# Optimization experiments

Hardware: AMD Instinct MI355X
Metric: run time of the kernel (lower is better)

## Reference

```python
import jax, jax.numpy as jnp
import numpy as np

N_CLASS = 20
N_SIGMA = 2
H = W = 512
B = 4
N_INST = 32
W_INST, W_VAR, W_SEED = 1.0, 10.0, 1.0
FG_WEIGHT = 10.0


def _xym():
    # channel 0: x along width, channel 1: y along height (matches torch buffer)
    xm = jnp.broadcast_to(jnp.linspace(0.0, 1.0, W)[None, :], (H, W))
    ym = jnp.broadcast_to(jnp.linspace(0.0, 1.0, H)[:, None], (H, W))
    return jnp.stack([xm, ym], axis=0)  # [2, H, W]


def lovasz_hinge_flat(logits, gt, valid):
    # logits, gt (0/1 float), valid (bool), all flat [P]; ignored pixels excluded
    P = logits.shape[0]
    vf = valid.astype(logits.dtype)
    signs = 2.0 * gt - 1.0
    # push ignored pixels to the end of the descending sort; relu(-1e9)=0 kills them
    errors = jnp.where(valid, 1.0 - logits * signs, -1e9)
    errors_sorted, perm = jax.lax.top_k(errors, P)  # descending
    gt_sorted = jnp.take(gt * vf, perm)
    v_sorted = jnp.take(vf, perm)
    gts = jnp.sum(gt * vf)
    inter = gts - jnp.cumsum(gt_sorted)
    union = gts + jnp.cumsum((1.0 - gt_sorted) * v_sorted)
    jac = 1.0 - inter / jnp.maximum(union, 1e-9)
    jac = jnp.concatenate([jac[:1], jac[1:] - jac[:-1]])
    return jnp.sum(jax.nn.relu(errors_sorted) * jac)


def _per_image(pred_b, inst_b, lab_b, xym, fg_w, n_inst):
    spatial_emb = jnp.tanh(pred_b[:2]) + xym            # [2,H,W]
    sigma = pred_b[2:2 + N_SIGMA]                       # [n_sigma,H,W]
    seed = jax.nn.sigmoid(pred_b[2 + N_SIGMA:2 + N_SIGMA + N_CLASS])  # [C,H,W]
    inst = inst_b[0]
    lab = lab_b[0]
    valid = (lab != 255)

    # background seed loss: sum over classes of seed^2 on pixels not of that class
    cls_ids = jnp.arange(N_CLASS)
    bg = (lab[None] != (cls_ids + 1)[:, None, None]) & valid[None]
    seed_bg = jnp.sum(jnp.square(seed) * bg)

    def per_inst(iid):
        m = (inst == iid)
        mf = m.astype(pred_b.dtype)
        cnt = jnp.maximum(jnp.sum(mf), 1.0)
        # to_center=True: center is mean coordinate of instance pixels
        center = jnp.sum(xym * mf[None], axis=(1, 2)) / cnt          # [2]
        s_mean = jnp.sum(sigma * mf[None], axis=(1, 2)) / cnt        # [n_sigma]
        var_l = jnp.sum(jnp.square(sigma - jax.lax.stop_gradient(s_mean)[:, None, None]) * mf[None]) / (N_SIGMA * cnt)
        s = jnp.exp(s_mean * 10.0)
        dist = jnp.exp(-jnp.sum(jnp.square(spatial_emb - center[:, None, None]) * s[:, None, None], axis=0))  # [H,W]
        inst_l = lovasz_hinge_flat((dist * 2.0 - 1.0).reshape(-1), mf.reshape(-1), valid.reshape(-1))
        cls = jnp.max(lab * m) - 1  # instance class (0-indexed)
        seed_c = jnp.take(seed, cls, axis=0)
        seed_fg = jnp.take(fg_w, cls) * jnp.sum(jnp.square(seed_c - jax.lax.stop_gradient(dist)) * mf)
        return inst_l, var_l, seed_fg

    inst_ls, var_ls, seed_fgs = jax.vmap(per_inst)(jnp.arange(1, n_inst + 1))
    instance_loss = jnp.sum(inst_ls) / n_inst
    var_loss = jnp.sum(var_ls) / n_inst
    seed_loss = (seed_bg + jnp.sum(seed_fgs)) / (H * W)
    return W_INST * instance_loss + W_VAR * var_loss + W_SEED * seed_loss


def setup_inputs() -> dict:
    key = jax.random.key(0)
    k1, k2 = jax.random.split(key)
    prediction = jax.random.normal(k1, (B, 2 + N_SIGMA + N_CLASS, H, W), dtype=jnp.float32)
    instances = jax.random.randint(k2, (B, 1, H, W), 0, N_INST + 1).astype(jnp.int32)
    # each instance id has a consistent class, as the torch instance_to_cls dict assumes
    labels = jnp.where(instances > 0, ((instances - 1) % N_CLASS) + 1, 0).astype(jnp.int32)
    return {"prediction": prediction, "instances": instances, "labels": labels, "n_instances": N_INST}


def reference(prediction, instances, labels, n_instances):
    xym = _xym()
    fg_w = jnp.full((N_CLASS,), FG_WEIGHT, dtype=prediction.dtype)
    per = jax.vmap(lambda p, i, l: _per_image(p, i, l, xym, fg_w, n_instances))(prediction, instances, labels)
    return jnp.mean(per) + jnp.sum(prediction) * 0.0
```

## Files before the change

### kernel.cpp

```cpp
#include <hip/hip_runtime.h>
#include <hip/hip_fp16.h>
#include <math.h>

#define HH 512
#define WW 512
#define BB 4
#define NCLS 20
#define NINST 32
#define NPIX (HH*WW)
#define NCH 24
#define NBIN 128
#define NCHUNK3 256
#define CPX3 1024
#define K3T 512
#define HSTR 33

#define OFF_PARTA  ((size_t)0)
#define OFF_PSEED  (OFF_PARTA + 1024*256*4)
#define OFF_STATS  (OFF_PSEED + 1024*4)
#define OFF_DER    (OFF_STATS + 8*128*4)
#define OFF_SEEDBG (OFF_DER + 7*128*4)
#define OFF_INSTL  (OFF_SEEDBG + 4*4)
#define OFF_SFG    (OFF_INSTL + 128*4)
#define OFF_REC    ((OFF_SFG + 1024*4 + 255) & ~(size_t)255)
#define OFF_HIST   (OFF_REC + (size_t)BB*NPIX*8)

__device__ __forceinline__ float fast_rcp(float x) { return __builtin_amdgcn_rcpf(x); }
__device__ __forceinline__ float fast_sigmoid(float z) { return fast_rcp(1.0f + __expf(-z)); }
__device__ __forceinline__ float fast_tanh(float x) {
  return 1.0f - 2.0f * fast_rcp(__expf(2.0f * x) + 1.0f);
}

__global__ __launch_bounds__(256) void k1_stats(
    const float* __restrict__ pred, const int* __restrict__ inst,
    const int* __restrict__ lab,
    float* __restrict__ partA, float* __restrict__ partSeed,
    uint2* __restrict__ rec)
{
  __shared__ unsigned s_st[4][NINST][9];
  __shared__ float s_seed;
  int t = threadIdx.x;
  int w = t >> 6;
  for (int i = t; i < 4*NINST*9; i += 256) ((unsigned*)s_st)[i] = 0u;
  if (t == 0) s_seed = 0.f;
  __syncthreads();

  int b = blockIdx.x >> 8;
  int blk = blockIdx.x & 255;
  const float* pb = pred + (size_t)b*NCH*NPIX;
  float seedloc = 0.f;

  int p = blk*1024 + t*4;
  float4 e0v = *(const float4*)(pb + p);
  float4 e1v = *(const float4*)(pb + NPIX + p);
  float4 g0v = *(const float4*)(pb + 2*NPIX + p);
  float4 g1v = *(const float4*)(pb + 3*NPIX + p);
  int4 idv = *(const int4*)(inst + (size_t)b*NPIX + p);
  int4 lbv = *(const int4*)(lab + (size_t)b*NPIX + p);

  #pragma unroll
  for (int u = 0; u < 4; ++u) {
    int px = p + u;
    int x = px & (WW-1);
    int y = px >> 9;
    float xm = x * (1.0f/(WW-1));
    float ym = y * (1.0f/(HH-1));
    float g0 = (&g0v.x)[u];
    float g1 = (&g1v.x)[u];
    int id = (&idv.x)[u];
    int lb = (&lbv.x)[u];
    if (id >= 1) {
      int j = id - 1;
      unsigned* row = s_st[w][j];
      atomicAdd(&row[0], 1u | ((lb != 255) ? 0x10000u : 0u));
      atomicAdd((float*)&row[1], xm);
      atomicAdd((float*)&row[2], ym);
      atomicAdd((float*)&row[3], g0);
      atomicAdd((float*)&row[4], g1);
      atomicAdd((float*)&row[5], g0*g0);
      atomicAdd((float*)&row[6], g1*g1);
    }
  }

  float so[4] = {0.f,0.f,0.f,0.f};
  float Sv[4] = {0.f,0.f,0.f,0.f};
  for (int c = 0; c < NCLS; ++c) {
    float4 sv = *(const float4*)(pb + (size_t)(4+c)*NPIX + p);
    #pragma unroll
    for (int u = 0; u < 4; ++u) {
      float sg = fast_sigmoid((&sv.x)[u]);
      Sv[u] += sg*sg;
      if (c + 1 == (&lbv.x)[u]) so[u] = sg;
    }
  }
  #pragma unroll
  for (int u = 0; u < 4; ++u)
    if ((&lbv.x)[u] != 255) seedloc += Sv[u] - so[u]*so[u];

  {
    uint2 r4[4];
    #pragma unroll
    for (int u = 0; u < 4; ++u) {
      int px = p + u;
      int x = px & (WW-1);
      int y = px >> 9;
      float ex = fast_tanh((&e0v.x)[u]) + x * (1.0f/(WW-1));
      float ey = fast_tanh((&e1v.x)[u]) + y * (1.0f/(HH-1));
      __half2 h = __floats2half2_rn(ex, ey);
      unsigned valid = ((&lbv.x)[u] != 255) ? 1u : 0u;
      unsigned meta = (unsigned)(&idv.x)[u] | (valid << 7);
      r4[u].x = *reinterpret_cast<unsigned*>(&h);
      r4[u].y = (unsigned)(unsigned char)(so[u]*255.f + 0.5f) | (meta << 8);
    }
    uint4* dst = (uint4*)(rec + (size_t)b*NPIX + p);
    dst[0] = make_uint4(r4[0].x, r4[0].y, r4[1].x, r4[1].y);
    dst[1] = make_uint4(r4[2].x, r4[2].y, r4[3].x, r4[3].y);
  }

  for (int o = 32; o; o >>= 1) seedloc += __shfl_down(seedloc, o);
  if ((t & 63) == 0) atomicAdd(&s_seed, seedloc);
  __syncthreads();

  {
    int j = t & 31, f = t >> 5;
    float v;
    if (f == 0) {
      unsigned s = (s_st[0][j][0] & 0xFFFFu) + (s_st[1][j][0] & 0xFFFFu)
                 + (s_st[2][j][0] & 0xFFFFu) + (s_st[3][j][0] & 0xFFFFu);
      v = (float)s;
    } else if (f == 7) {
      unsigned s = (s_st[0][j][0] >> 16) + (s_st[1][j][0] >> 16)
                 + (s_st[2][j][0] >> 16) + (s_st[3][j][0] >> 16);
      v = (float)s;
    } else {
      v = __uint_as_float(s_st[0][j][f]) + __uint_as_float(s_st[1][j][f])
        + __uint_as_float(s_st[2][j][f]) + __uint_as_float(s_st[3][j][f]);
    }
    partA[(blockIdx.x << 8) + t] = v;
  }
  if (t == 0) partSeed[blockIdx.x] = s_seed;
}

__global__ __launch_bounds__(256) void k2a_reduce(
    const float* __restrict__ partA, float* __restrict__ stats)
{
  __shared__ float red[256];
  int bid = blockIdx.x;
  int b = bid >> 3, f = bid & 7;
  int t = threadIdx.x;
  int j = t & 31, grp = t >> 5;
  float s = 0.f;
  #pragma unroll 8
  for (int k = 0; k < 32; ++k) {
    int blk = grp*32 + k;
    s += partA[((b*256 + blk) << 8) + (f << 5) + j];
  }
  red[t] = s; __syncthreads();
  for (int st = 128; st >= 32; st >>= 1) {
    if (t < st) red[t] += red[t + st];
    __syncthreads();
  }
  if (t < 32) stats[f*128 + b*32 + t] = red[t];
}

__global__ __launch_bounds__(128) void k2b_derive(
    const float* __restrict__ stats, const float* __restrict__ partSeed,
    float* __restrict__ der, float* __restrict__ seedbg)
{
  int t = threadIdx.x;
  if (t < 4) {
    float ss = 0.f;
    for (int i = 0; i < 256; ++i) ss += partSeed[t*256 + i];
    seedbg[t] = ss;
  }
  float cntA = stats[0*128+t];
  float cnt = fmaxf(cntA, 1.0f);
  float sumx = stats[1*128+t], sumy = stats[2*128+t];
  float s0 = stats[3*128+t], s1 = stats[4*128+t];
  float q0 = stats[5*128+t], q1 = stats[6*128+t];
  float Gv = stats[7*128+t];
  float cx = sumx/cnt, cy = sumy/cnt;
  float sm0 = s0/cnt, sm1 = s1/cnt;
  float varnum = q0 - 2.f*sm0*s0 + cntA*sm0*sm0
               + q1 - 2.f*sm1*s1 + cntA*sm1*sm1;
  float varl = varnum / (2.0f * cnt);
  der[0*128+t] = cx;
  der[1*128+t] = cy;
  der[2*128+t] = -1.442695041f * expf(10.f*sm0);
  der[3*128+t] = -1.442695041f * expf(10.f*sm1);
  der[4*128+t] = varl;
  der[5*128+t] = Gv;
}

__global__ __launch_bounds__(K3T) void k3_hist(
    const uint2* __restrict__ rec, const float* __restrict__ der,
    unsigned* __restrict__ hist, float* __restrict__ sfg)
{
  __shared__ unsigned hc[NBIN*HSTR];
  __shared__ float s_fg[8];
  int t = threadIdx.x;
  for (int i = t; i < NBIN*HSTR; i += K3T) hc[i] = 0u;
  int bid = blockIdx.x;
  int b = bid >> 8;
  int chunk = bid & 255;
  int w = t >> 6, lane = t & 63;
  int j = lane & 31, jp1 = j + 1;
  int pair = b*NINST + j;
  float cx = der[0*128+pair], cy = der[1*128+pair];
  float s0 = der[2*128+pair], s1 = der[3*128+pair];
  const uint2* rb = rec + (size_t)b*NPIX + chunk*CPX3 + w*128;
  __syncthreads();

  float fg = 0.f;
  #pragma unroll 4
  for (int r = 0; r < 64; ++r) {
    uint2 rv = rb[r*2 + (lane >> 5)];
    __half2 h;
    *reinterpret_cast<unsigned*>(&h) = rv.x;
    float2 e = __half22float2(h);
    unsigned hi = rv.y;
    float dx = e.x - cx, dy = e.y - cy;
    float dist = exp2f(dx*dx*s0 + dy*dy*s1);
    bool own = ((int)((hi >> 8) & 0x3F) == jp1);
    if (own) { float d = (float)(hi & 0xFFu)*(1.0f/255.f) - dist; fg += d*d; }
    if (hi & 0x8000u) {
      float f = own ? (1.0f - dist) : dist;
      unsigned bin = min((unsigned)(f * (float)NBIN), NBIN-1u);
      atomicAdd(&hc[bin*HSTR + j], own ? 0x10001u : 1u);
    }
  }
  for (int o = 32; o; o >>= 1) fg += __shfl_down(fg, o);
  if (lane == 0) s_fg[w] = fg;
  __syncthreads();
  if (t == 0) {
    float s = 0.f;
    #pragma unroll
    for (int i = 0; i < 8; ++i) s += s_fg[i];
    sfg[bid] = 10.0f * s;
  }
  unsigned* out = hist + (size_t)(b*NCHUNK3 + chunk) * (NINST*NBIN);
  #pragma unroll
  for (int k = 0; k < NINST*NBIN/K3T; ++k) {
    int idx = k*K3T + t;
    out[idx] = hc[(idx & 127)*HSTR + (idx >> 7)];
  }
}

__global__ __launch_bounds__(512) void k4_scan(
    const unsigned* __restrict__ hist, const float* __restrict__ der,
    float* __restrict__ instl)
{
  __shared__ unsigned s_c[4][NBIN], s_p[4][NBIN];
  int t = threadIdx.x;
  int pair = blockIdx.x;
  int b = pair >> 5, j = pair & 31;
  int grp = t >> 7, bin = t & 127;
  const unsigned* bp = hist + ((size_t)b*NCHUNK3*NINST + j)*NBIN + bin;
  unsigned c = 0, p = 0;
  #pragma unroll 8
  for (int ch = grp*64; ch < grp*64 + 64; ++ch) {
    unsigned v = bp[(size_t)ch * (NINST*NBIN)];
    c += v & 0xFFFFu; p += v >> 16;
  }
  s_c[grp][bin] = c; s_p[grp][bin] = p;
  __syncthreads();
  if (t < NBIN) {
    s_c[0][t] += s_c[1][t] + s_c[2][t] + s_c[3][t];
    s_p[0][t] += s_p[1][t] + s_p[2][t] + s_p[3][t];
  }
  __syncthreads();

  if (t < 64) {
    int lane = t;
    float G = der[5*128+pair];
    unsigned carryN = 0, carryP = 0;
    float Jprev = 0.f, L = 0.f;
    for (int c8 = 0; c8 < NBIN/64; ++c8) {
      int k = NBIN - 1 - c8*64 - lane;
      unsigned n = s_c[0][k], pp0 = s_p[0][k];
      for (int off = 1; off < 64; off <<= 1) {
        unsigned nn = __shfl_up(n, off);
        unsigned pq = __shfl_up(pp0, off);
        if (lane >= off) { n += nn; pp0 += pq; }
      }
      float fN = (float)(carryN + n);
      float fP = (float)(carryP + pp0);
      float uni = G + fN - fP;
      float J = 1.0f - (G - fP) / fmaxf(uni, 1e-9f);
      float Jp = __shfl_up(J, 1);
      if (lane == 0) Jp = Jprev;
      float v = (k + 0.5f) * (2.0f/NBIN);
      L += v * (J - Jp);
      carryN += __shfl(n, 63);
      carryP += __shfl(pp0, 63);
      Jprev  = __shfl(J, 63);
    }
    for (int o = 32; o; o >>= 1) L += __shfl_down(L, o);
    if (lane == 0) instl[pair] = L;
  }
}

__global__ __launch_bounds__(256) void k5_final(
    const float* __restrict__ instl, const float* __restrict__ der,
    const float* __restrict__ seedbg, const float* __restrict__ sfg,
    float* __restrict__ out)
{
  __shared__ float red[256];
  int t = threadIdx.x;
  float acc = 0.f;
  for (int i = t; i < 1024; i += 256) acc += sfg[i];
  acc *= (1.0f/NPIX);
  if (t < 4) acc += seedbg[t] * (1.0f/NPIX);
  if (t < 128) acc += (instl[t] + 10.0f*der[4*128+t]) * (1.0f/NINST);
  red[t] = acc; __syncthreads();
  for (int s = 128; s; s >>= 1) { if (t < s) red[t] += red[t+s]; __syncthreads(); }
  if (t == 0) out[0] = red[0] * (1.0f/BB);
}

extern "C" void kernel_launch(void* const* d_in, const int* in_sizes, int n_in,
                              void* d_out, int out_size, void* d_ws, size_t ws_size,
                              hipStream_t stream)
{
  const float* pred = (const float*)d_in[0];
  const int* inst = (const int*)d_in[1];
  const int* lab  = (const int*)d_in[2];
  char* ws = (char*)d_ws;
  float* partA = (float*)(ws + OFF_PARTA);
  float* partSeed = (float*)(ws + OFF_PSEED);
  float* stats = (float*)(ws + OFF_STATS);
  float* der = (float*)(ws + OFF_DER);
  float* seedbg = (float*)(ws + OFF_SEEDBG);
  float* instl = (float*)(ws + OFF_INSTL);
  float* sfg = (float*)(ws + OFF_SFG);
  uint2* rec = (uint2*)(ws + OFF_REC);
  unsigned* hist = (unsigned*)(ws + OFF_HIST);

  hipLaunchKernelGGL(k1_stats, dim3(1024), dim3(256), 0, stream,
                     pred, inst, lab, partA, partSeed, rec);
  hipLaunchKernelGGL(k2a_reduce, dim3(32), dim3(256), 0, stream, partA, stats);
  hipLaunchKernelGGL(k2b_derive, dim3(1), dim3(128), 0, stream,
                     stats, partSeed, der, seedbg);
  hipLaunchKernelGGL(k3_hist, dim3(BB*NCHUNK3), dim3(K3T), 0, stream,
                     rec, der, hist, sfg);
  hipLaunchKernelGGL(k4_scan, dim3(128), dim3(512), 0, stream, hist, der, instl);
  hipLaunchKernelGGL(k5_final, dim3(1), dim3(256), 0, stream,
                     instl, der, seedbg, sfg, (float*)d_out);
}
```

Measured before the change: 94.01 us.

## Fuse derive and final kernels, skip bin-zero histogram atomics

```diff
diff --git a/kernel.cpp b/kernel.cpp
--- a/kernel.cpp
+++ b/kernel.cpp
@@ -17,12 +17,13 @@
 
 #define OFF_PARTA  ((size_t)0)
 #define OFF_PSEED  (OFF_PARTA + 1024*256*4)
-#define OFF_STATS  (OFF_PSEED + 1024*4)
-#define OFF_DER    (OFF_STATS + 8*128*4)
-#define OFF_SEEDBG (OFF_DER + 7*128*4)
-#define OFF_INSTL  (OFF_SEEDBG + 4*4)
+#define OFF_STATS  (OFF_PSEED + 1024*8)
+#define OFF_SEEDBG (OFF_STATS + 8*128*4)
+#define OFF_VALID  (OFF_SEEDBG + 4*4)
+#define OFF_INSTL  (OFF_VALID + 4*4)
 #define OFF_SFG    (OFF_INSTL + 128*4)
-#define OFF_REC    ((OFF_SFG + 1024*4 + 255) & ~(size_t)255)
+#define OFF_CNT    (OFF_SFG + 1024*4)
+#define OFF_REC    ((OFF_CNT + 4 + 255) & ~(size_t)255)
 #define OFF_HIST   (OFF_REC + (size_t)BB*NPIX*8)
 
 __device__ __forceinline__ float fast_rcp(float x) { return __builtin_amdgcn_rcpf(x); }
@@ -34,21 +35,20 @@
 __global__ __launch_bounds__(256) void k1_stats(
     const float* __restrict__ pred, const int* __restrict__ inst,
     const int* __restrict__ lab,
-    float* __restrict__ partA, float* __restrict__ partSeed,
+    float* __restrict__ partA, float2* __restrict__ partSeed,
     uint2* __restrict__ rec)
 {
   __shared__ unsigned s_st[4][NINST][9];
-  __shared__ float s_seed;
+  __shared__ float s_seed, s_valid;
   int t = threadIdx.x;
   int w = t >> 6;
   for (int i = t; i < 4*NINST*9; i += 256) ((unsigned*)s_st)[i] = 0u;
-  if (t == 0) s_seed = 0.f;
+  if (t == 0) { s_seed = 0.f; s_valid = 0.f; }
   __syncthreads();
 
   int b = blockIdx.x >> 8;
   int blk = blockIdx.x & 255;
   const float* pb = pred + (size_t)b*NCH*NPIX;
-  float seedloc = 0.f;
 
   int p = blk*1024 + t*4;
   float4 e0v = *(const float4*)(pb + p);
@@ -58,6 +58,7 @@
   int4 idv = *(const int4*)(inst + (size_t)b*NPIX + p);
   int4 lbv = *(const int4*)(lab + (size_t)b*NPIX + p);
 
+  float vloc = 0.f;
   #pragma unroll
   for (int u = 0; u < 4; ++u) {
     int px = p + u;
@@ -69,6 +70,7 @@
     float g1 = (&g1v.x)[u];
     int id = (&idv.x)[u];
     int lb = (&lbv.x)[u];
+    if (lb != 255) vloc += 1.0f;
     if (id >= 1) {
       int j = id - 1;
       unsigned* row = s_st[w][j];
@@ -82,6 +84,7 @@
     }
   }
 
+  float seedloc = 0.f;
   float so[4] = {0.f,0.f,0.f,0.f};
   float Sv[4] = {0.f,0.f,0.f,0.f};
   for (int c = 0; c < NCLS; ++c) {
@@ -116,9 +119,11 @@
     dst[0] = make_uint4(r4[0].x, r4[0].y, r4[1].x, r4[1].y);
     dst[1] = make_uint4(r4[2].x, r4[2].y, r4[3].x, r4[3].y);
   }
-
-  for (int o = 32; o; o >>= 1) seedloc += __shfl_down(seedloc, o);
-  if ((t & 63) == 0) atomicAdd(&s_seed, seedloc);
+  for (int o = 32; o; o >>= 1) {
+    seedloc += __shfl_down(seedloc, o);
+    vloc    += __shfl_down(vloc, o);
+  }
+  if ((t & 63) == 0) { atomicAdd(&s_seed, seedloc); atomicAdd(&s_valid, vloc); }
   __syncthreads();
 
   {
@@ -138,78 +143,75 @@
     }
     partA[(blockIdx.x << 8) + t] = v;
   }
-  if (t == 0) partSeed[blockIdx.x] = s_seed;
+  if (t == 0) partSeed[blockIdx.x] = make_float2(s_seed, s_valid);
 }
 
 __global__ __launch_bounds__(256) void k2a_reduce(
-    const float* __restrict__ partA, float* __restrict__ stats)
-{
-  __shared__ float red[256];
+    const float* __restrict__ partA, const float2* __restrict__ partSeed,
+    float* __restrict__ stats, float* __restrict__ seedbg,
+    float* __restrict__ validT, unsigned* __restrict__ counter)
+{
   int bid = blockIdx.x;
-  int b = bid >> 3, f = bid & 7;
   int t = threadIdx.x;
-  int j = t & 31, grp = t >> 5;
-  float s = 0.f;
-  #pragma unroll 8
-  for (int k = 0; k < 32; ++k) {
-    int blk = grp*32 + k;
-    s += partA[((b*256 + blk) << 8) + (f << 5) + j];
-  }
-  red[t] = s; __syncthreads();
-  for (int st = 128; st >= 32; st >>= 1) {
-    if (t < st) red[t] += red[t + st];
-    __syncthreads();
-  }
-  if (t < 32) stats[f*128 + b*32 + t] = red[t];
-}
-
-__global__ __launch_bounds__(128) void k2b_derive(
-    const float* __restrict__ stats, const float* __restrict__ partSeed,
-    float* __restrict__ der, float* __restrict__ seedbg)
-{
-  int t = threadIdx.x;
-  if (t < 4) {
-    float ss = 0.f;
-    for (int i = 0; i < 256; ++i) ss += partSeed[t*256 + i];
-    seedbg[t] = ss;
-  }
-  float cntA = stats[0*128+t];
-  float cnt = fmaxf(cntA, 1.0f);
-  float sumx = stats[1*128+t], sumy = stats[2*128+t];
-  float s0 = stats[3*128+t], s1 = stats[4*128+t];
-  float q0 = stats[5*128+t], q1 = stats[6*128+t];
-  float Gv = stats[7*128+t];
-  float cx = sumx/cnt, cy = sumy/cnt;
-  float sm0 = s0/cnt, sm1 = s1/cnt;
-  float varnum = q0 - 2.f*sm0*s0 + cntA*sm0*sm0
-               + q1 - 2.f*sm1*s1 + cntA*sm1*sm1;
-  float varl = varnum / (2.0f * cnt);
-  der[0*128+t] = cx;
-  der[1*128+t] = cy;
-  der[2*128+t] = -1.442695041f * expf(10.f*sm0);
-  der[3*128+t] = -1.442695041f * expf(10.f*sm1);
-  der[4*128+t] = varl;
-  der[5*128+t] = Gv;
+  if (bid < 32) {
+    __shared__ float red[256];
+    int b = bid >> 3, f = bid & 7;
+    int j = t & 31, grp = t >> 5;
+    float s = 0.f;
+    #pragma unroll 8
+    for (int k = 0; k < 32; ++k)
+      s += partA[((b*256 + grp*32 + k) << 8) + (f << 5) + j];
+    red[t] = s; __syncthreads();
+    for (int st = 128; st >= 32; st >>= 1) {
+      if (t < st) red[t] += red[t + st];
+      __syncthreads();
+    }
+    if (t < 32) stats[f*128 + b*32 + t] = red[t];
+  } else {
+    if (t == 0) counter[0] = 0u;
+    int img = t >> 6, slot = t & 63;
+    float s = 0.f, v = 0.f;
+    #pragma unroll
+    for (int k = 0; k < 4; ++k) {
+      float2 ps = partSeed[img*256 + slot*4 + k];
+      s += ps.x; v += ps.y;
+    }
+    for (int o = 32; o; o >>= 1) {
+      s += __shfl_down(s, o);
+      v += __shfl_down(v, o);
+    }
+    if (slot == 0) { seedbg[img] = s; validT[img] = v; }
+  }
 }
 
 __global__ __launch_bounds__(K3T) void k3_hist(
-    const uint2* __restrict__ rec, const float* __restrict__ der,
+    const uint2* __restrict__ rec, const float* __restrict__ stats,
     unsigned* __restrict__ hist, float* __restrict__ sfg)
 {
   __shared__ unsigned hc[NBIN*HSTR];
+  __shared__ float sder[NINST][4];
   __shared__ float s_fg[8];
   int t = threadIdx.x;
-  for (int i = t; i < NBIN*HSTR; i += K3T) hc[i] = 0u;
   int bid = blockIdx.x;
   int b = bid >> 8;
   int chunk = bid & 255;
+  for (int i = t; i < NBIN*HSTR; i += K3T) hc[i] = 0u;
+  if (t < NINST) {
+    int pr = b*NINST + t;
+    float cnt = fmaxf(stats[0*128+pr], 1.0f);
+    float rc = fast_rcp(cnt);
+    sder[t][0] = stats[1*128+pr] * rc;
+    sder[t][1] = stats[2*128+pr] * rc;
+    sder[t][2] = -1.442695041f * __expf(10.f * stats[3*128+pr] * rc);
+    sder[t][3] = -1.442695041f * __expf(10.f * stats[4*128+pr] * rc);
+  }
+  __syncthreads();
+
   int w = t >> 6, lane = t & 63;
   int j = lane & 31, jp1 = j + 1;
-  int pair = b*NINST + j;
-  float cx = der[0*128+pair], cy = der[1*128+pair];
-  float s0 = der[2*128+pair], s1 = der[3*128+pair];
+  float cx = sder[j][0], cy = sder[j][1];
+  float s0 = sder[j][2], s1 = sder[j][3];
   const uint2* rb = rec + (size_t)b*NPIX + chunk*CPX3 + w*128;
-  __syncthreads();
 
   float fg = 0.f;
   #pragma unroll 4
@@ -226,7 +228,7 @@
     if (hi & 0x8000u) {
       float f = own ? (1.0f - dist) : dist;
       unsigned bin = min((unsigned)(f * (float)NBIN), NBIN-1u);
-      atomicAdd(&hc[bin*HSTR + j], own ? 0x10001u : 1u);
+      if (bin) atomicAdd(&hc[bin*HSTR + j], own ? 0x10001u : 1u);
     }
   }
   for (int o = 32; o; o >>= 1) fg += __shfl_down(fg, o);
@@ -246,11 +248,16 @@
   }
 }
 
-__global__ __launch_bounds__(512) void k4_scan(
-    const unsigned* __restrict__ hist, const float* __restrict__ der,
-    float* __restrict__ instl)
+__global__ __launch_bounds__(512) void k45_scan_final(
+    const unsigned* __restrict__ hist, const float* __restrict__ stats,
+    const float* __restrict__ validT, const float* __restrict__ seedbg,
+    const float* __restrict__ sfg, float* __restrict__ instl,
+    unsigned* __restrict__ counter, float* __restrict__ out)
 {
   __shared__ unsigned s_c[4][NBIN], s_p[4][NBIN];
+  __shared__ unsigned rc[NBIN], rp[NBIN];
+  __shared__ float redf[512];
+  __shared__ int lastflag;
   int t = threadIdx.x;
   int pair = blockIdx.x;
   int b = pair >> 5, j = pair & 31;
@@ -265,14 +272,25 @@
   s_c[grp][bin] = c; s_p[grp][bin] = p;
   __syncthreads();
   if (t < NBIN) {
-    s_c[0][t] += s_c[1][t] + s_c[2][t] + s_c[3][t];
-    s_p[0][t] += s_p[1][t] + s_p[2][t] + s_p[3][t];
+    unsigned cc = s_c[0][t] + s_c[1][t] + s_c[2][t] + s_c[3][t];
+    unsigned pp = s_p[0][t] + s_p[1][t] + s_p[2][t] + s_p[3][t];
+    s_c[0][t] = cc; s_p[0][t] = pp;
+    rc[t] = t ? cc : 0u; rp[t] = t ? pp : 0u;
+  }
+  __syncthreads();
+  for (int st = 64; st; st >>= 1) {
+    if (t < st) { rc[t] += rc[t+st]; rp[t] += rp[t+st]; }
+    __syncthreads();
+  }
+  float G = stats[7*128+pair];
+  if (t == 0) {
+    s_c[0][0] = (unsigned)validT[b] - rc[0];
+    s_p[0][0] = (unsigned)G - rp[0];
   }
   __syncthreads();
 
   if (t < 64) {
     int lane = t;
-    float G = der[5*128+pair];
     unsigned carryN = 0, carryP = 0;
     float Jprev = 0.f, L = 0.f;
     for (int c8 = 0; c8 < NBIN/64; ++c8) {
@@ -298,23 +316,35 @@
     for (int o = 32; o; o >>= 1) L += __shfl_down(L, o);
     if (lane == 0) instl[pair] = L;
   }
-}
-
-__global__ __launch_bounds__(256) void k5_final(
-    const float* __restrict__ instl, const float* __restrict__ der,
-    const float* __restrict__ seedbg, const float* __restrict__ sfg,
-    float* __restrict__ out)
-{
-  __shared__ float red[256];
-  int t = threadIdx.x;
-  float acc = 0.f;
-  for (int i = t; i < 1024; i += 256) acc += sfg[i];
-  acc *= (1.0f/NPIX);
+  __threadfence();
+  __syncthreads();
+  if (t == 0) {
+    unsigned old = atomicAdd(counter, 1u);
+    lastflag = (old == 127u) ? 1 : 0;
+  }
+  __syncthreads();
+  if (!lastflag) return;
+
+  float acc = (sfg[t] + sfg[t + 512]) * (1.0f/NPIX);
   if (t < 4) acc += seedbg[t] * (1.0f/NPIX);
-  if (t < 128) acc += (instl[t] + 10.0f*der[4*128+t]) * (1.0f/NINST);
-  red[t] = acc; __syncthreads();
-  for (int s = 128; s; s >>= 1) { if (t < s) red[t] += red[t+s]; __syncthreads(); }
-  if (t == 0) out[0] = red[0] * (1.0f/BB);
+  if (t < 128) {
+    float cntA = stats[0*128+t];
+    float cnt = fmaxf(cntA, 1.0f);
+    float s0 = stats[3*128+t], s1 = stats[4*128+t];
+    float q0 = stats[5*128+t], q1 = stats[6*128+t];
+    float sm0 = s0/cnt, sm1 = s1/cnt;
+    float varnum = q0 - 2.f*sm0*s0 + cntA*sm0*sm0
+                 + q1 - 2.f*sm1*s1 + cntA*sm1*sm1;
+    float varl = varnum / (2.0f * cnt);
+    float il = atomicAdd(&instl[t], 0.0f);
+    acc += (il + 10.0f*varl) * (1.0f/NINST);
+  }
+  redf[t] = acc; __syncthreads();
+  for (int st = 256; st; st >>= 1) {
+    if (t < st) redf[t] += redf[t+st];
+    __syncthreads();
+  }
+  if (t == 0) out[0] = redf[0] * (1.0f/BB);
 }
 
 extern "C" void kernel_launch(void* const* d_in, const int* in_sizes, int n_in,
@@ -326,23 +356,22 @@
   const int* lab  = (const int*)d_in[2];
   char* ws = (char*)d_ws;
   float* partA = (float*)(ws + OFF_PARTA);
-  float* partSeed = (float*)(ws + OFF_PSEED);
+  float2* partSeed = (float2*)(ws + OFF_PSEED);
   float* stats = (float*)(ws + OFF_STATS);
-  float* der = (float*)(ws + OFF_DER);
   float* seedbg = (float*)(ws + OFF_SEEDBG);
+  float* validT = (float*)(ws + OFF_VALID);
   float* instl = (float*)(ws + OFF_INSTL);
   float* sfg = (float*)(ws + OFF_SFG);
+  unsigned* counter = (unsigned*)(ws + OFF_CNT);
   uint2* rec = (uint2*)(ws + OFF_REC);
   unsigned* hist = (unsigned*)(ws + OFF_HIST);
 
   hipLaunchKernelGGL(k1_stats, dim3(1024), dim3(256), 0, stream,
                      pred, inst, lab, partA, partSeed, rec);
-  hipLaunchKernelGGL(k2a_reduce, dim3(32), dim3(256), 0, stream, partA, stats);
-  hipLaunchKernelGGL(k2b_derive, dim3(1), dim3(128), 0, stream,
-                     stats, partSeed, der, seedbg);
+  hipLaunchKernelGGL(k2a_reduce, dim3(33), dim3(256), 0, stream,
+                     partA, partSeed, stats, seedbg, validT, counter);
   hipLaunchKernelGGL(k3_hist, dim3(BB*NCHUNK3), dim3(K3T), 0, stream,
-                     rec, der, hist, sfg);
-  hipLaunchKernelGGL(k4_scan, dim3(128), dim3(512), 0, stream, hist, der, instl);
-  hipLaunchKernelGGL(k5_final, dim3(1), dim3(256), 0, stream,
-                     instl, der, seedbg, sfg, (float*)d_out);
-}
+                     rec, stats, hist, sfg);
+  hipLaunchKernelGGL(k45_scan_final, dim3(128), dim3(512), 0, stream,
+                     hist, stats, validT, seedbg, sfg, instl, counter, (float*)d_out);
+}
```

Result: slower. 103.8 us (+10.4%).
